# Optimization experiments

Measured on AMD Instinct MI355X. Metric: run time of the kernel, lower is better.

Reference implementation:

```python
import jax, jax.numpy as jnp
import numpy as np

B, V, M, C = 1024, 2, 256, 256  # batch, num_vars (must be 2), latent states, categories


def setup_inputs() -> dict:
    key = jax.random.key(0)
    k1, k2, k3 = jax.random.split(key, 3)
    x = jax.random.randint(k1, (B, V), 0, C)
    # input-node tables: per var v, per latent node k, a [M, C] row-normalized table
    W = jax.nn.softmax(jax.random.normal(k2, (V, M, M, C), dtype=jnp.float32), axis=-1)
    # sum-node mixture weights over the M product children
    w_sum = jax.nn.softmax(jax.random.normal(k3, (M,), dtype=jnp.float32))
    return {"x": x, "W": W, "w_sum": w_sum}


def reference(x, W, w_sum):
    # lp[v] has shape [M(k), M(m), B]: log W[v, k, m, x[b, v]]
    # (matches torch: probs[:, x_var].log() per input node, stacked over latent k)
    lp0 = jnp.log(W[0][:, :, x[:, 0]])  # [M, M, B]
    lp1 = jnp.log(W[1][:, :, x[:, 1]])  # [M, M, B]
    prod = lp0 + lp1                    # product nodes, [M(k), M, B]
    # sum node: log( sum_k w_k * exp(prod_k) ) -> [M, B]
    mixed = jnp.log(jnp.einsum('k,kmb->mb', w_sum, jnp.exp(prod)))
    # root: logsumexp over the leading M dim -> [B]
    return jax.nn.logsumexp(mixed, axis=0)
```

## Files before the change

kernel.cpp:

```cpp
#include <hip/hip_runtime.h>
#include <math.h>


#define SPLITS  256
#define KCHUNK  256
#define BK      32
#define NITER   (KCHUNK / BK)
#define LDSS    40

typedef float  f32x4  __attribute__((ext_vector_type(4)));
typedef short  bf16x8 __attribute__((ext_vector_type(8)));

static __device__ __forceinline__ short f2bf(float f) {
    unsigned u = __builtin_bit_cast(unsigned, f);
    u += 0x7fffu + ((u >> 16) & 1u);
    return (short)(u >> 16);
}

template <bool USE_PART>
__global__ __launch_bounds__(512, 2) void gemm_s_kernel(
    const float* __restrict__ W, const float* __restrict__ wsum,
    float* __restrict__ out_acc)
{
    __shared__ short As[2][256 * LDSS];
    __shared__ short Bs[2][256 * LDSS];

    const int  split = blockIdx.x;
    const long kbase = (long)split * KCHUNK;
    const float wk   = wsum[split];

    const float* __restrict__ Ag = W + kbase * 256;
    const float* __restrict__ Bg = W + 16777216 + kbase * 256;

    const int t  = threadIdx.x;
    const int cq = (t & 63) * 4;
    const int kq = (t >> 6) * 4;

    const int lane = t & 63;
    const int wv   = t >> 6;
    const int wc0  = (wv & 3) * 64;
    const int wc1  = (wv >> 2) * 128;
    const int ml   = lane & 15;
    const int qd   = lane >> 4;

    f32x4 acc[4][8];
#pragma unroll
    for (int i = 0; i < 4; ++i)
#pragma unroll
        for (int j = 0; j < 8; ++j) acc[i][j] = (f32x4){0.f, 0.f, 0.f, 0.f};

    float4 a4[4], b4[4];

#pragma unroll
    for (int r = 0; r < 4; ++r) {
        a4[r] = *(const float4*)(Ag + (long)(kq + r) * 256 + cq);
        b4[r] = *(const float4*)(Bg + (long)(kq + r) * 256 + cq);
    }
    {
        const float* af32 = reinterpret_cast<const float*>(a4);
        const float* bf32 = reinterpret_cast<const float*>(b4);
#pragma unroll
        for (int j = 0; j < 4; ++j) {
            short4 av, bv;
            av.x = f2bf(af32[0 * 4 + j] * wk);
            av.y = f2bf(af32[1 * 4 + j] * wk);
            av.z = f2bf(af32[2 * 4 + j] * wk);
            av.w = f2bf(af32[3 * 4 + j] * wk);
            bv.x = f2bf(bf32[0 * 4 + j]);
            bv.y = f2bf(bf32[1 * 4 + j]);
            bv.z = f2bf(bf32[2 * 4 + j]);
            bv.w = f2bf(bf32[3 * 4 + j]);
            *(short4*)&As[0][(cq + j) * LDSS + kq] = av;
            *(short4*)&Bs[0][(cq + j) * LDSS + kq] = bv;
        }
    }
    __syncthreads();

#pragma unroll
    for (int it = 0; it < NITER; ++it) {
        const int cur = it & 1;
        if (it + 1 < NITER) {
#pragma unroll
            for (int r = 0; r < 4; ++r) {
                a4[r] = *(const float4*)(Ag + (long)((it + 1) * BK + kq + r) * 256 + cq);
                b4[r] = *(const float4*)(Bg + (long)((it + 1) * BK + kq + r) * 256 + cq);
            }
        }
        bf16x8 afr[4];
#pragma unroll
        for (int mi = 0; mi < 4; ++mi)
            afr[mi] = *(const bf16x8*)&As[cur][(wc0 + mi * 16 + ml) * LDSS + qd * 8];
#pragma unroll
        for (int ni = 0; ni < 8; ++ni) {
            const bf16x8 bfr = *(const bf16x8*)&Bs[cur][(wc1 + ni * 16 + ml) * LDSS + qd * 8];
#pragma unroll
            for (int mi = 0; mi < 4; ++mi)
                acc[mi][ni] = __builtin_amdgcn_mfma_f32_16x16x32_bf16(
                    afr[mi], bfr, acc[mi][ni], 0, 0, 0);
        }
        if (it + 1 < NITER) {
            const float* af32 = reinterpret_cast<const float*>(a4);
            const float* bf32 = reinterpret_cast<const float*>(b4);
#pragma unroll
            for (int j = 0; j < 4; ++j) {
                short4 av, bv;
                av.x = f2bf(af32[0 * 4 + j] * wk);
                av.y = f2bf(af32[1 * 4 + j] * wk);
                av.z = f2bf(af32[2 * 4 + j] * wk);
                av.w = f2bf(af32[3 * 4 + j] * wk);
                bv.x = f2bf(bf32[0 * 4 + j]);
                bv.y = f2bf(bf32[1 * 4 + j]);
                bv.z = f2bf(bf32[2 * 4 + j]);
                bv.w = f2bf(bf32[3 * 4 + j]);
                *(short4*)&As[1 - cur][(cq + j) * LDSS + kq] = av;
                *(short4*)&Bs[1 - cur][(cq + j) * LDSS + kq] = bv;
            }
            __syncthreads();
        }
    }

    if (USE_PART) {
        float* __restrict__ Pb = out_acc + (size_t)split * 65536;
#pragma unroll
        for (int mi = 0; mi < 4; ++mi) {
            const int row0 = wc0 + mi * 16 + qd * 4;
#pragma unroll
            for (int ni = 0; ni < 8; ++ni) {
                const int col = wc1 + ni * 16 + ml;
#pragma unroll
                for (int r = 0; r < 4; ++r)
                    Pb[(row0 + r) * 256 + col] = acc[mi][ni][r];
            }
        }
    } else {
#pragma unroll
        for (int mi = 0; mi < 4; ++mi) {
            const int row0 = wc0 + mi * 16 + qd * 4;
#pragma unroll
            for (int ni = 0; ni < 8; ++ni) {
                const int col = wc1 + ni * 16 + ml;
#pragma unroll
                for (int r = 0; r < 4; ++r)
                    atomicAdd(&out_acc[(row0 + r) * 256 + col], acc[mi][ni][r]);
            }
        }
    }
}

__global__ __launch_bounds__(64) void finish_part_kernel(
    const int* __restrict__ x, const float* __restrict__ P, float* __restrict__ out)
{
    const int b  = blockIdx.x;
    const int t  = threadIdx.x;
    const int x0 = x[2 * b], x1 = x[2 * b + 1];
    const size_t base = (size_t)x0 * 256 + x1;
    float v = 0.f;
#pragma unroll
    for (int j = 0; j < 4; ++j)
        v += P[(size_t)(t + 64 * j) * 65536 + base];
#pragma unroll
    for (int off = 32; off > 0; off >>= 1) v += __shfl_down(v, off);
    if (t == 0) out[b] = logf(v);
}

__global__ __launch_bounds__(64) void finish_atom_kernel(
    const int* __restrict__ x, const float* __restrict__ S, float* __restrict__ out)
{
    const int b  = blockIdx.x * 64 + threadIdx.x;
    const int x0 = x[2 * b], x1 = x[2 * b + 1];
    out[b] = logf(S[x0 * 256 + x1]);
}

extern "C" void kernel_launch(void* const* d_in, const int* in_sizes, int n_in,
                              void* d_out, int out_size, void* d_ws, size_t ws_size,
                              hipStream_t stream)
{
    const int*   x    = (const int*)d_in[0];
    const float* W    = (const float*)d_in[1];
    const float* wsum = (const float*)d_in[2];
    float* out = (float*)d_out;

    const size_t part_bytes = (size_t)SPLITS * 65536 * sizeof(float);

    if (ws_size >= part_bytes) {
        float* P = (float*)d_ws;
        gemm_s_kernel<true><<<dim3(SPLITS), 512, 0, stream>>>(W, wsum, P);
        finish_part_kernel<<<dim3(1024), 64, 0, stream>>>(x, P, out);
    } else {
        float* S = (float*)d_ws;
        hipMemsetAsync(d_ws, 0, 65536 * sizeof(float), stream);
        gemm_s_kernel<false><<<dim3(SPLITS), 512, 0, stream>>>(W, wsum, S);
        finish_atom_kernel<<<dim3(16), 64, 0, stream>>>(x, S, out);
    }
}
```

Before: 211.5 us.

## Fuse gather and log into GEMM epilogue with per-batch atomics and last-block finish

```diff
diff --git a/kernel.cpp b/kernel.cpp
--- a/kernel.cpp
+++ b/kernel.cpp
@@ -17,13 +17,18 @@
     return (short)(u >> 16);
 }
 
-template <bool USE_PART>
-__global__ __launch_bounds__(512, 2) void gemm_s_kernel(
-    const float* __restrict__ W, const float* __restrict__ wsum,
-    float* __restrict__ out_acc)
+__global__ __launch_bounds__(512, 2) void hclt_fused_kernel(
+    const int* __restrict__ x, const float* __restrict__ W,
+    const float* __restrict__ wsum, float* __restrict__ S_b,
+    int* __restrict__ counter, float* __restrict__ out)
 {
-    __shared__ short As[2][256 * LDSS];
-    __shared__ short Bs[2][256 * LDSS];
+    __shared__ __align__(16) char smem[81920];
+    __shared__ int pairs[1024];
+    __shared__ int lastFlag;
+
+    short* const AsB[2] = { (short*)smem,           (short*)(smem + 20480) };
+    short* const BsB[2] = { (short*)(smem + 40960), (short*)(smem + 61440) };
+    float* const gat    = (float*)smem;
 
     const int  split = blockIdx.x;
     const long kbase = (long)split * KCHUNK;
@@ -42,6 +47,13 @@
     const int wc1  = (wv >> 2) * 128;
     const int ml   = lane & 15;
     const int qd   = lane >> 4;
+
+    {
+        const int2 x0 = ((const int2*)x)[t];
+        const int2 x1 = ((const int2*)x)[t + 512];
+        pairs[t]       = (x0.x << 8) | x0.y;
+        pairs[t + 512] = (x1.x << 8) | x1.y;
+    }
 
     f32x4 acc[4][8];
 #pragma unroll
@@ -70,8 +82,8 @@
             bv.y = f2bf(bf32[1 * 4 + j]);
             bv.z = f2bf(bf32[2 * 4 + j]);
             bv.w = f2bf(bf32[3 * 4 + j]);
-            *(short4*)&As[0][(cq + j) * LDSS + kq] = av;
-            *(short4*)&Bs[0][(cq + j) * LDSS + kq] = bv;
+            *(short4*)&AsB[0][(cq + j) * LDSS + kq] = av;
+            *(short4*)&BsB[0][(cq + j) * LDSS + kq] = bv;
         }
     }
     __syncthreads();
@@ -89,10 +101,10 @@
         bf16x8 afr[4];
 #pragma unroll
         for (int mi = 0; mi < 4; ++mi)
-            afr[mi] = *(const bf16x8*)&As[cur][(wc0 + mi * 16 + ml) * LDSS + qd * 8];
+            afr[mi] = *(const bf16x8*)&AsB[cur][(wc0 + mi * 16 + ml) * LDSS + qd * 8];
 #pragma unroll
         for (int ni = 0; ni < 8; ++ni) {
-            const bf16x8 bfr = *(const bf16x8*)&Bs[cur][(wc1 + ni * 16 + ml) * LDSS + qd * 8];
+            const bf16x8 bfr = *(const bf16x8*)&BsB[cur][(wc1 + ni * 16 + ml) * LDSS + qd * 8];
 #pragma unroll
             for (int mi = 0; mi < 4; ++mi)
                 acc[mi][ni] = __builtin_amdgcn_mfma_f32_16x16x32_bf16(
@@ -112,63 +124,56 @@
                 bv.y = f2bf(bf32[1 * 4 + j]);
                 bv.z = f2bf(bf32[2 * 4 + j]);
                 bv.w = f2bf(bf32[3 * 4 + j]);
-                *(short4*)&As[1 - cur][(cq + j) * LDSS + kq] = av;
-                *(short4*)&Bs[1 - cur][(cq + j) * LDSS + kq] = bv;
+                *(short4*)&AsB[1 - cur][(cq + j) * LDSS + kq] = av;
+                *(short4*)&BsB[1 - cur][(cq + j) * LDSS + kq] = bv;
             }
             __syncthreads();
         }
     }
 
-    if (USE_PART) {
-        float* __restrict__ Pb = out_acc + (size_t)split * 65536;
+    const int myphase = wv >> 1, mybuf = wv & 1;
+#pragma unroll 1
+    for (int ph = 0; ph < 4; ++ph) {
+        __syncthreads();
+        if (myphase == ph) {
+            float* dst = gat + mybuf * 8256;
 #pragma unroll
-        for (int mi = 0; mi < 4; ++mi) {
-            const int row0 = wc0 + mi * 16 + qd * 4;
+            for (int mi = 0; mi < 4; ++mi)
 #pragma unroll
-            for (int ni = 0; ni < 8; ++ni) {
-                const int col = wc1 + ni * 16 + ml;
+                for (int ni = 0; ni < 8; ++ni)
 #pragma unroll
-                for (int r = 0; r < 4; ++r)
-                    Pb[(row0 + r) * 256 + col] = acc[mi][ni][r];
-            }
+                    for (int r = 0; r < 4; ++r)
+                        dst[(mi * 16 + qd * 4 + r) * 129 + (ni * 16 + ml)] = acc[mi][ni][r];
         }
-    } else {
+        __syncthreads();
 #pragma unroll
-        for (int mi = 0; mi < 4; ++mi) {
-            const int row0 = wc0 + mi * 16 + qd * 4;
-#pragma unroll
-            for (int ni = 0; ni < 8; ++ni) {
-                const int col = wc1 + ni * 16 + ml;
-#pragma unroll
-                for (int r = 0; r < 4; ++r)
-                    atomicAdd(&out_acc[(row0 + r) * 256 + col], acc[mi][ni][r]);
+        for (int i = t; i < 1024; i += 512) {
+            const int pr = pairs[i];
+            const int c0 = pr >> 8, c1 = pr & 255;
+            const int own = (c0 >> 6) | ((c1 >> 7) << 2);
+            if ((own >> 1) == ph) {
+                const float v = gat[(own & 1) * 8256 + (c0 & 63) * 129 + (c1 & 127)];
+#if defined(__gfx950__) || defined(__AMDGCN__)
+                unsafeAtomicAdd(&S_b[i], v);
+#else
+                atomicAdd(&S_b[i], v);
+#endif
             }
         }
     }
-}
 
-__global__ __launch_bounds__(64) void finish_part_kernel(
-    const int* __restrict__ x, const float* __restrict__ P, float* __restrict__ out)
-{
-    const int b  = blockIdx.x;
-    const int t  = threadIdx.x;
-    const int x0 = x[2 * b], x1 = x[2 * b + 1];
-    const size_t base = (size_t)x0 * 256 + x1;
-    float v = 0.f;
+    __threadfence();
+    if (t == 0) lastFlag = (atomicAdd(counter, 1) == SPLITS - 1);
+    __syncthreads();
+    if (lastFlag) {
+        __threadfence();
 #pragma unroll
-    for (int j = 0; j < 4; ++j)
-        v += P[(size_t)(t + 64 * j) * 65536 + base];
-#pragma unroll
-    for (int off = 32; off > 0; off >>= 1) v += __shfl_down(v, off);
-    if (t == 0) out[b] = logf(v);
-}
-
-__global__ __launch_bounds__(64) void finish_atom_kernel(
-    const int* __restrict__ x, const float* __restrict__ S, float* __restrict__ out)
-{
-    const int b  = blockIdx.x * 64 + threadIdx.x;
-    const int x0 = x[2 * b], x1 = x[2 * b + 1];
-    out[b] = logf(S[x0 * 256 + x1]);
+        for (int i = t; i < 1024; i += 512) {
+            const float s = __hip_atomic_load(&S_b[i], __ATOMIC_RELAXED,
+                                              __HIP_MEMORY_SCOPE_AGENT);
+            out[i] = logf(s);
+        }
+    }
 }
 
 extern "C" void kernel_launch(void* const* d_in, const int* in_sizes, int n_in,
@@ -180,16 +185,9 @@
     const float* wsum = (const float*)d_in[2];
     float* out = (float*)d_out;
 
-    const size_t part_bytes = (size_t)SPLITS * 65536 * sizeof(float);
+    float* S_b     = (float*)d_ws;
+    int*   counter = (int*)d_ws + 1024;
 
-    if (ws_size >= part_bytes) {
-        float* P = (float*)d_ws;
-        gemm_s_kernel<true><<<dim3(SPLITS), 512, 0, stream>>>(W, wsum, P);
-        finish_part_kernel<<<dim3(1024), 64, 0, stream>>>(x, P, out);
-    } else {
-        float* S = (float*)d_ws;
-        hipMemsetAsync(d_ws, 0, 65536 * sizeof(float), stream);
-        gemm_s_kernel<false><<<dim3(SPLITS), 512, 0, stream>>>(W, wsum, S);
-        finish_atom_kernel<<<dim3(16), 64, 0, stream>>>(x, S, out);
-    }
+    hipMemsetAsync(d_ws, 0, 1024 * sizeof(float) + sizeof(int), stream);
+    hclt_fused_kernel<<<dim3(SPLITS), 512, 0, stream>>>(x, W, wsum, S_b, counter, out);
 }
```

Measured after the change: 247.4 us. 1.17x slower.
